# Kernel tuning notes

Hardware: AMD Instinct MI355X
Metric: run time of the kernel (lower is better)

The kernel has to match this reference:

```python
import jax, jax.numpy as jnp
import numpy as np


def setup_inputs() -> dict:
    key = jax.random.key(0)
    ks = jax.random.split(key, 4)
    L, B, T, H, D = 12, 4, 2048, 16, 64
    current_layer = jax.random.normal(ks[0], (B, T, H, D), dtype=jnp.float32)
    all_layers = jax.random.normal(ks[1], (L, B, T, H, D), dtype=jnp.float32)
    # nn.init.normal_(std=0.02) for both projections
    Wq = jax.random.normal(ks[2], (D, D), dtype=jnp.float32) * 0.02
    Wk = jax.random.normal(ks[3], (D, D), dtype=jnp.float32) * 0.02
    scales = jnp.full((L,), 1.0 / L, dtype=jnp.float32)  # LayerScalingFactor init 1/num_layers
    temperature = jnp.ones((1,), dtype=jnp.float32)
    return {
        "current_layer": current_layer,
        "all_layers": all_layers,
        "Wq": Wq,
        "Wk": Wk,
        "scales": scales,
        "temperature": temperature,
        "current_layer_idx": 0,
    }


def reference(current_layer, all_layers, Wq, Wk, scales, temperature, current_layer_idx):
    # current_layer: [B,T,H,D]; all_layers: [L,B,T,H,D] (stack of per-layer outputs)
    # num_heads = 1, so per-head dim == D and scores are over the layer axis L.
    D = current_layer.shape[-1]
    q = jnp.einsum("bthd,ed->bthe", current_layer, Wq)          # query_proj (no bias)
    k = jnp.einsum("lbthd,ed->lbthe", all_layers, Wk)           # key_proj (no bias)
    inv_scale = 1.0 / (jnp.sqrt(jnp.asarray(D, q.dtype)) * jnp.abs(temperature[0]))
    scores = jnp.einsum("bthd,lbthd->bthl", q, k) * inv_scale   # [B,T,H,L]
    attn = jax.nn.softmax(scores, axis=-1)
    attn = attn * scales                                        # per-layer learned scale
    attn = attn / (jnp.sum(attn, axis=-1, keepdims=True) + 1e-6)  # renormalize
    # per-layer accumulation: output += scales[l] * attn[...,l] * all_layers[l]
    out = jnp.einsum("bthl,l,lbthd->bthd", attn, scales, all_layers)
    return out
```

## Files before the change

### kernel.cpp

```cpp
#include <hip/hip_runtime.h>
#include <hip/hip_bf16.h>

constexpr int L = 12;
constexpr int B = 4, T = 2048, H = 16, D = 64;
constexpr int NPOS = B * T * H;
constexpr long long SLAYER = (long long)NPOS * D;
constexpr int PW = 16;

typedef __attribute__((ext_vector_type(8))) short bf16x8;
typedef __attribute__((ext_vector_type(4))) float f32x4;

__device__ __forceinline__ short f2bf(float f) {
  union { __hip_bfloat16 h; short s; } u;
  u.h = __float2bfloat16(f);
  return u.s;
}

__global__ __launch_bounds__(64) void cla_precompute_MT(
    const float* __restrict__ Wq, const float* __restrict__ Wk,
    short* __restrict__ MT) {
  const int n = blockIdx.x;
  const int k = threadIdx.x;
  float acc = 0.f;
  #pragma unroll
  for (int e = 0; e < D; ++e)
    acc = fmaf(Wq[e * D + k], Wk[e * D + n], acc);
  MT[n * D + k] = f2bf(acc);
}

template <int CTRL, int ROWM>
__device__ __forceinline__ float dpp_add(float x) {
  int moved = __builtin_amdgcn_update_dpp(0, __float_as_int(x), CTRL, ROWM, 0xF,
                                          false);
  return x + __int_as_float(moved);
}
__device__ __forceinline__ float wave_sum_bcast(float x) {
  x = dpp_add<0x111, 0xF>(x);
  x = dpp_add<0x112, 0xF>(x);
  x = dpp_add<0x114, 0xF>(x);
  x = dpp_add<0x118, 0xF>(x);
  x = dpp_add<0x142, 0xA>(x);
  x = dpp_add<0x143, 0xC>(x);
  return __int_as_float(__builtin_amdgcn_readlane(__float_as_int(x), 63));
}

__global__ __launch_bounds__(256, 8) void cla_main(
    const float* __restrict__ cur, const float* __restrict__ all,
    const short* __restrict__ MT, const float* __restrict__ scales,
    const float* __restrict__ temperature, float* __restrict__ out) {
  __shared__ float qlds[4][PW * D];

  const int lane = threadIdx.x & 63;
  const int w    = threadIdx.x >> 6;
  const int wid  = blockIdx.x * 4 + w;
  const int pos0 = wid * PW;

  const int ncol = lane & 15;
  const int kq   = lane >> 4;

  const float inv_scale = 1.0f / (8.0f * fabsf(temperature[0]));

  bf16x8 af[2];
  {
    const float* xb = cur + (size_t)(pos0 + ncol) * D + kq * 8;
    #pragma unroll
    for (int kc = 0; kc < 2; ++kc) {
      const float4 xlo = *(const float4*)(xb + kc * 32);
      const float4 xhi = *(const float4*)(xb + kc * 32 + 4);
      short a8[8] = {f2bf(xlo.x), f2bf(xlo.y), f2bf(xlo.z), f2bf(xlo.w),
                     f2bf(xhi.x), f2bf(xhi.y), f2bf(xhi.z), f2bf(xhi.w)};
      __builtin_memcpy(&af[kc], a8, 16);
    }
  }

  #pragma unroll
  for (int nt = 0; nt < 4; ++nt) {
    f32x4 acc = {};
    #pragma unroll
    for (int kc = 0; kc < 2; ++kc) {
      const bf16x8 bm =
          *(const bf16x8*)(MT + (nt * 16 + ncol) * D + kc * 32 + kq * 8);
      acc = __builtin_amdgcn_mfma_f32_16x16x32_bf16(af[kc], bm, acc, 0, 0, 0);
    }
    #pragma unroll
    for (int r = 0; r < 4; ++r)
      qlds[w][(4 * kq + r) * D + nt * 16 + ncol] = acc[r] * inv_scale;
  }

  for (int it = 0; it < PW; ++it) {
    const size_t pbase = (size_t)(pos0 + it) * D;
    const float q = qlds[w][it * D + lane];

    float y[L];
    #pragma unroll
    for (int l = 0; l < L; ++l) {
      const float* p = all + (size_t)l * SLAYER + pbase;
      y[l] = p[lane];
    }

    float sc[L];
    #pragma unroll
    for (int l = 0; l < L; ++l)
      sc[l] = wave_sum_bcast(q * y[l]);

    float mx = sc[0];
    #pragma unroll
    for (int l = 1; l < L; ++l) mx = fmaxf(mx, sc[l]);
    float sum = 0.f;
    #pragma unroll
    for (int l = 0; l < L; ++l) { sc[l] = __expf(sc[l] - mx); sum += sc[l]; }
    const float inv_sum = 1.0f / sum;

    float ssum = 0.f;
    #pragma unroll
    for (int l = 0; l < L; ++l) {
      sc[l] = sc[l] * inv_sum * scales[l];
      ssum += sc[l];
    }
    const float r = 1.0f / (ssum + 1e-6f);

    float o = 0.f;
    #pragma unroll
    for (int l = 0; l < L; ++l) o = fmaf(sc[l] * r * scales[l], y[l], o);

    out[pbase + lane] = o;
  }
}

extern "C" void kernel_launch(void* const* d_in, const int* in_sizes, int n_in,
                              void* d_out, int out_size, void* d_ws, size_t ws_size,
                              hipStream_t stream) {
  const float* cur    = (const float*)d_in[0];
  const float* all    = (const float*)d_in[1];
  const float* Wq     = (const float*)d_in[2];
  const float* Wk     = (const float*)d_in[3];
  const float* scales = (const float*)d_in[4];
  const float* temp   = (const float*)d_in[5];
  short* MT = (short*)d_ws;

  cla_precompute_MT<<<64, 64, 0, stream>>>(Wq, Wk, MT);

  const int nwaves  = NPOS / PW;
  const int nblocks = nwaves / 4;
  cla_main<<<nblocks, 256, 0, stream>>>(cur, all, MT, scales, temp,
                                        (float*)d_out);
}
```

Baseline: 113.9 us.

## Restructure main loop with vectorized loads, online softmax, and double-buffered layer groups

```diff
diff --git a/kernel.cpp b/kernel.cpp
--- a/kernel.cpp
+++ b/kernel.cpp
@@ -6,6 +6,7 @@
 constexpr int NPOS = B * T * H;
 constexpr long long SLAYER = (long long)NPOS * D;
 constexpr int PW = 16;
+constexpr int NG = 3, GL = 4;
 
 typedef __attribute__((ext_vector_type(8))) short bf16x8;
 typedef __attribute__((ext_vector_type(4))) float f32x4;
@@ -28,23 +29,21 @@
   MT[n * D + k] = f2bf(acc);
 }
 
-template <int CTRL, int ROWM>
-__device__ __forceinline__ float dpp_add(float x) {
-  int moved = __builtin_amdgcn_update_dpp(0, __float_as_int(x), CTRL, ROWM, 0xF,
+template <int CTRL>
+__device__ __forceinline__ float ror_add(float x) {
+  int moved = __builtin_amdgcn_update_dpp(0, __float_as_int(x), CTRL, 0xF, 0xF,
                                           false);
   return x + __int_as_float(moved);
 }
-__device__ __forceinline__ float wave_sum_bcast(float x) {
-  x = dpp_add<0x111, 0xF>(x);
-  x = dpp_add<0x112, 0xF>(x);
-  x = dpp_add<0x114, 0xF>(x);
-  x = dpp_add<0x118, 0xF>(x);
-  x = dpp_add<0x142, 0xA>(x);
-  x = dpp_add<0x143, 0xC>(x);
-  return __int_as_float(__builtin_amdgcn_readlane(__float_as_int(x), 63));
-}
-
-__global__ __launch_bounds__(256, 8) void cla_main(
+__device__ __forceinline__ float row_sum16(float x) {
+  x = ror_add<0x121>(x);
+  x = ror_add<0x122>(x);
+  x = ror_add<0x124>(x);
+  x = ror_add<0x128>(x);
+  return x;
+}
+
+__global__ __launch_bounds__(256, 2) void cla_main(
     const float* __restrict__ cur, const float* __restrict__ all,
     const short* __restrict__ MT, const float* __restrict__ scales,
     const float* __restrict__ temperature, float* __restrict__ out) {
@@ -54,9 +53,19 @@
   const int w    = threadIdx.x >> 6;
   const int wid  = blockIdx.x * 4 + w;
   const int pos0 = wid * PW;
-
   const int ncol = lane & 15;
   const int kq   = lane >> 4;
+
+  const size_t sbase = (size_t)pos0 * D + (size_t)lane * 4;
+
+  float4 yb[2][GL][4];
+  #pragma unroll
+  for (int i = 0; i < GL; ++i) {
+    const float* p = all + (size_t)i * SLAYER + sbase;
+    #pragma unroll
+    for (int t = 0; t < 4; ++t)
+      yb[0][i][t] = *(const float4*)(p + t * 256);
+  }
 
   const float inv_scale = 1.0f / (8.0f * fabsf(temperature[0]));
 
@@ -72,7 +81,6 @@
       __builtin_memcpy(&af[kc], a8, 16);
     }
   }
-
   #pragma unroll
   for (int nt = 0; nt < 4; ++nt) {
     f32x4 acc = {};
@@ -87,43 +95,92 @@
       qlds[w][(4 * kq + r) * D + nt * 16 + ncol] = acc[r] * inv_scale;
   }
 
-  for (int it = 0; it < PW; ++it) {
-    const size_t pbase = (size_t)(pos0 + it) * D;
-    const float q = qlds[w][it * D + lane];
-
-    float y[L];
-    #pragma unroll
-    for (int l = 0; l < L; ++l) {
-      const float* p = all + (size_t)l * SLAYER + pbase;
-      y[l] = p[lane];
-    }
-
-    float sc[L];
-    #pragma unroll
-    for (int l = 0; l < L; ++l)
-      sc[l] = wave_sum_bcast(q * y[l]);
-
-    float mx = sc[0];
-    #pragma unroll
-    for (int l = 1; l < L; ++l) mx = fmaxf(mx, sc[l]);
-    float sum = 0.f;
-    #pragma unroll
-    for (int l = 0; l < L; ++l) { sc[l] = __expf(sc[l] - mx); sum += sc[l]; }
-    const float inv_sum = 1.0f / sum;
-
-    float ssum = 0.f;
-    #pragma unroll
-    for (int l = 0; l < L; ++l) {
-      sc[l] = sc[l] * inv_sum * scales[l];
-      ssum += sc[l];
-    }
-    const float r = 1.0f / (ssum + 1e-6f);
-
-    float o = 0.f;
-    #pragma unroll
-    for (int l = 0; l < L; ++l) o = fmaf(sc[l] * r * scales[l], y[l], o);
-
-    out[pbase + lane] = o;
+  const int gq = lane >> 4;
+  const int j  = lane & 15;
+  float4 q[4];
+  #pragma unroll
+  for (int t = 0; t < 4; ++t)
+    q[t] = *(const float4*)&qlds[w][(t * 4 + gq) * D + 4 * j];
+
+  float scl[L], scl2[L];
+  #pragma unroll
+  for (int l = 0; l < L; ++l) {
+    scl[l]  = scales[l];
+    scl2[l] = scl[l] * scl[l];
+  }
+
+  float m[4], S[4], A[4];
+  f32x4 N[4];
+  #pragma unroll
+  for (int t = 0; t < 4; ++t) {
+    m[t] = -3.0e38f;
+    S[t] = 0.f;
+    A[t] = 0.f;
+    N[t] = (f32x4){0.f, 0.f, 0.f, 0.f};
+  }
+
+  #pragma unroll
+  for (int gi = 0; gi < NG; ++gi) {
+    if (gi + 1 < NG) {
+      #pragma unroll
+      for (int i = 0; i < GL; ++i) {
+        const float* p = all + (size_t)((gi + 1) * GL + i) * SLAYER + sbase;
+        #pragma unroll
+        for (int t = 0; t < 4; ++t)
+          yb[(gi + 1) & 1][i][t] = *(const float4*)(p + t * 256);
+      }
+    }
+
+    #pragma unroll
+    for (int t = 0; t < 4; ++t) {
+      float sc[GL];
+      #pragma unroll
+      for (int i = 0; i < GL; ++i) {
+        const float4 y = yb[gi & 1][i][t];
+        const float s =
+            q[t].x * y.x + q[t].y * y.y + q[t].z * y.z + q[t].w * y.w;
+        sc[i] = row_sum16(s);
+      }
+      float gm = sc[0];
+      #pragma unroll
+      for (int i = 1; i < GL; ++i) gm = fmaxf(gm, sc[i]);
+      const float mn = fmaxf(m[t], gm);
+      const float c  = __expf(m[t] - mn);
+      m[t] = mn;
+
+      float e[GL];
+      float dS = 0.f, dA = 0.f;
+      #pragma unroll
+      for (int i = 0; i < GL; ++i) {
+        e[i] = __expf(sc[i] - mn);
+        dS += e[i];
+        dA += scl[gi * GL + i] * e[i];
+      }
+      S[t] = S[t] * c + dS;
+      A[t] = A[t] * c + dA;
+
+      float ax = 0.f, ay = 0.f, az = 0.f, aw = 0.f;
+      #pragma unroll
+      for (int i = 0; i < GL; ++i) {
+        const float wl = scl2[gi * GL + i] * e[i];
+        const float4 y = yb[gi & 1][i][t];
+        ax = fmaf(wl, y.x, ax);
+        ay = fmaf(wl, y.y, ay);
+        az = fmaf(wl, y.z, az);
+        aw = fmaf(wl, y.w, aw);
+      }
+      N[t][0] = N[t][0] * c + ax;
+      N[t][1] = N[t][1] * c + ay;
+      N[t][2] = N[t][2] * c + az;
+      N[t][3] = N[t][3] * c + aw;
+    }
+  }
+
+  #pragma unroll
+  for (int t = 0; t < 4; ++t) {
+    const float r = 1.0f / (A[t] + 1e-6f * S[t]);
+    *(float4*)(out + sbase + t * 256) =
+        make_float4(N[t][0] * r, N[t][1] * r, N[t][2] * r, N[t][3] * r);
   }
 }
 
```

After: 100.6 us. -11.7%, faster.
